# Optimization experiments

Measured on AMD Instinct MI355X. Metric: run time of the kernel, lower is better.

Reference implementation:

```python
import jax, jax.numpy as jnp
import numpy as np

IMG = 640
C = 80
K = 10
LB, LC = 7.5, 0.5
ALPHA_COST, BETA_COST = 0.5, 6.0
GAMMA, ALPHA = 2.0, 0.25
EPS = 1e-7
PI = 3.141592653589793


def xywh_to_xyxy(b):
    cx, cy, w, h = b[..., 0], b[..., 1], b[..., 2], b[..., 3]
    return jnp.stack([cx - w * 0.5, cy - h * 0.5, cx + w * 0.5, cy + h * 0.5], axis=-1)


def bbox_iou(box1, box2):
    # box1 [M,4], box2 [N,4] xyxy -> [M,N]
    area1 = jnp.clip(box1[:, 2] - box1[:, 0], 0) * jnp.clip(box1[:, 3] - box1[:, 1], 0)
    area2 = jnp.clip(box2[:, 2] - box2[:, 0], 0) * jnp.clip(box2[:, 3] - box2[:, 1], 0)
    ix1 = jnp.maximum(box1[:, None, 0], box2[None, :, 0])
    iy1 = jnp.maximum(box1[:, None, 1], box2[None, :, 1])
    ix2 = jnp.minimum(box1[:, None, 2], box2[None, :, 2])
    iy2 = jnp.minimum(box1[:, None, 3], box2[None, :, 3])
    inter = jnp.clip(ix2 - ix1, 0) * jnp.clip(iy2 - iy1, 0)
    union = area1[:, None] + area2[None, :] - inter + EPS
    return jnp.clip(inter / union, 0.0, 1.0)


def bbox_ciou(p, t):
    # elementwise [N,4] x [N,4] xyxy -> [N]
    px1, py1, px2, py2 = p[:, 0], p[:, 1], p[:, 2], p[:, 3]
    tx1, ty1, tx2, ty2 = t[:, 0], t[:, 1], t[:, 2], t[:, 3]
    pw = jnp.clip(px2 - px1, EPS)
    ph = jnp.clip(py2 - py1, EPS)
    tw = jnp.clip(tx2 - tx1, EPS)
    th = jnp.clip(ty2 - ty1, EPS)
    inter = jnp.clip(jnp.minimum(px2, tx2) - jnp.maximum(px1, tx1), 0) * \
            jnp.clip(jnp.minimum(py2, ty2) - jnp.maximum(py1, ty1), 0)
    union = pw * ph + tw * th - inter + EPS
    iou = inter / union
    cd = ((px1 + px2) * 0.5 - (tx1 + tx2) * 0.5) ** 2 + ((py1 + py2) * 0.5 - (ty1 + ty2) * 0.5) ** 2
    cw = jnp.maximum(px2, tx2) - jnp.minimum(px1, tx1)
    ch = jnp.maximum(py2, ty2) - jnp.minimum(py1, ty1)
    c2 = cw ** 2 + ch ** 2 + EPS
    v = (4.0 / PI ** 2) * (jnp.arctan(tw / th) - jnp.arctan(pw / ph)) ** 2
    alpha = jax.lax.stop_gradient(v / (v - iou + 1.0 + EPS))
    return iou - cd / c2 - alpha * v


def _decode(p, stride):
    # p: [B, A, S, S, E] -> box [B, A*S*S, 4] (xywh px), cls [B, A*S*S, C]
    B, A, S, _, E = p.shape
    tx, ty, tw, th = p[..., 0], p[..., 1], p[..., 2], p[..., 3]
    gy, gx = jnp.meshgrid(jnp.arange(S, dtype=p.dtype), jnp.arange(S, dtype=p.dtype), indexing='ij')
    gx = gx.reshape(1, 1, S, S)
    gy = gy.reshape(1, 1, S, S)
    px = (jax.nn.sigmoid(tx) * 2.0 - 0.5 + gx) * stride  # center_mode='v8'
    py = (jax.nn.sigmoid(ty) * 2.0 - 0.5 + gy) * stride
    pw = jax.nn.softplus(tw) * stride                      # wh_mode='softplus'
    ph = jax.nn.softplus(th) * stride
    box = jnp.stack([px, py, pw, ph], axis=-1).reshape(B, -1, 4)
    cls = p[..., 4:].reshape(B, -1, C)
    return box, cls


def _per_image(p_box, p_logits, gt, labels):
    # p_box [M,4] xywh, p_logits [M,C], gt [N,4] xyxy, labels [N]
    N = gt.shape[0]
    tcx = (gt[:, 0] + gt[:, 2]) * 0.5
    tcy = (gt[:, 1] + gt[:, 3]) * 0.5
    dist = (p_box[:, 0][:, None] - tcx[None, :]) ** 2 + (p_box[:, 1][:, None] - tcy[None, :]) ** 2  # [M,N]
    _, cand = jax.lax.top_k(-dist.T, K)       # [N,K] nearest anchors per target
    cand = cand.reshape(-1)                    # [N*K] (dups don't change the min)
    cand_box = p_box[cand]
    cand_logits = p_logits[cand]
    cls_score = jax.nn.sigmoid(cand_logits)[:, labels]          # [NK,N]
    iou = bbox_iou(xywh_to_xyxy(cand_box), gt)                  # [NK,N]
    cost = ALPHA_COST * (1.0 - cls_score) + BETA_COST * (1.0 - iou)
    matched = cand[jnp.argmin(cost, axis=0)]                    # [N]
    ciou = bbox_ciou(xywh_to_xyxy(p_box[matched]), gt)
    loss_box = LB * jnp.sum(1.0 - ciou) / N
    tgt = jnp.zeros_like(p_logits).at[matched, labels].set(1.0)  # [M,C]
    x = p_logits
    ce = jnp.maximum(x, 0) - x * tgt + jnp.log1p(jnp.exp(-jnp.abs(x)))
    pr = jax.nn.sigmoid(x)
    p_t = pr * tgt + (1 - pr) * (1 - tgt)
    fl = ce * (1 - p_t) ** GAMMA
    a_t = ALPHA * tgt + (1 - ALPHA) * (1 - tgt)
    loss_cls = LC * jnp.sum(a_t * fl) / N
    return loss_box + loss_cls


def _forward(p0, p1, p2, gt_boxes, labels):
    boxes, logits = [], []
    for p in (p0, p1, p2):
        S = p.shape[2]
        pb, pl = _decode(p, float(IMG) / S)
        boxes.append(pb)
        logits.append(pl)
    flat_boxes = jnp.concatenate(boxes, axis=1)    # [B, 8400, 4]
    flat_logits = jnp.concatenate(logits, axis=1)  # [B, 8400, C]
    per_img = jax.vmap(_per_image)(flat_boxes, flat_logits, gt_boxes, labels)  # [B]
    return jnp.mean(per_img)


def setup_inputs() -> dict:
    key = jax.random.key(0)
    k0, k1, k2, kc, kw, kl = jax.random.split(key, 6)
    B, N = 16, 60
    p0 = jax.random.normal(k0, (B, 1, 80, 80, 84), dtype=jnp.float32)
    p1 = jax.random.normal(k1, (B, 1, 40, 40, 84), dtype=jnp.float32)
    p2 = jax.random.normal(k2, (B, 1, 20, 20, 84), dtype=jnp.float32)
    c = jax.random.uniform(kc, (B, N, 2), minval=64.0, maxval=576.0)
    wh = jax.random.uniform(kw, (B, N, 2), minval=8.0, maxval=128.0)
    gt_boxes = jnp.concatenate([c - wh * 0.5, c + wh * 0.5], axis=-1).astype(jnp.float32)
    labels = jax.random.randint(kl, (B, N), 0, 80, dtype=jnp.int32)
    return {"p0": p0, "p1": p1, "p2": p2, "gt_boxes": gt_boxes, "labels": labels}


def reference(p0, p1, p2, gt_boxes, labels):
    return _forward(p0, p1, p2, gt_boxes, labels)
```

## Files before the change

### kernel.cpp

```cpp
#include <hip/hip_runtime.h>
#include <cfloat>
#include <math.h>

#define NB   16
#define NGT  60
#define NA   8400
#define KNN  10
#define NCAND (NGT*KNN)
#define EPSF 1e-7f
#define PIF  3.14159265358979f
#define FOCAL_BLOCKS 2048
#define TOPK_BLOCKS  240

#define NV0   2150400u
#define NV1    537600u
#define NV2    134400u
#define FOCAL_COUNT 2688000u

#define LOG2E 1.44269504088896341f
#define LN2   0.69314718055994531f

__device__ __forceinline__ float fexp2(float x){ return __builtin_amdgcn_exp2f(x); }
__device__ __forceinline__ float flog2(float x){ return __builtin_amdgcn_logf(x); }
__device__ __forceinline__ float frcp (float x){ return __builtin_amdgcn_rcpf(x); }

__device__ __forceinline__ float fsigm(float x){
  return frcp(1.0f + fexp2(-x*LOG2E));
}
__device__ __forceinline__ float fsoftplus(float x){
  float u = fexp2(-fabsf(x)*LOG2E);
  return fmaxf(x,0.f) + LN2*flog2(1.0f + u);
}
__device__ __forceinline__ float fbg(float x){
  float u = fexp2(fminf(-x*LOG2E, 126.0f));
  float t = frcp(1.0f + u);
  return (x + LN2*flog2(1.0f + u)) * t * t;
}

struct ARow { const float* q; float stf; int i, j; };
__device__ __forceinline__ ARow anchor_row(const float* p0,const float* p1,const float* p2,int img,int a){
  ARow r;
  if (a < 6400){ int l=a;      r.q = p0 + (size_t)(img*6400 + l)*84; r.stf= 8.f; r.i=l/80; r.j=l-80*r.i; }
  else if (a < 8000){ int l=a-6400; r.q = p1 + (size_t)(img*1600 + l)*84; r.stf=16.f; r.i=l/40; r.j=l-40*r.i; }
  else { int l=a-8000;         r.q = p2 + (size_t)(img*400  + l)*84; r.stf=32.f; r.i=l/20; r.j=l-20*r.i; }
  return r;
}
__device__ __forceinline__ float4 decode_box_xywh(const ARow& r){
  float4 x4 = *(const float4*)r.q;
  float px = (fsigm(x4.x)*2.f - 0.5f + (float)r.j)*r.stf;
  float py = (fsigm(x4.y)*2.f - 0.5f + (float)r.i)*r.stf;
  float pw = fsoftplus(x4.z)*r.stf;
  float ph = fsoftplus(x4.w)*r.stf;
  return make_float4(px,py,pw,ph);
}

__global__ __launch_bounds__(256) void focal_topk_kernel(const float* __restrict__ p0,
                                                         const float* __restrict__ p1,
                                                         const float* __restrict__ p2,
                                                         const float* __restrict__ gt,
                                                         int* __restrict__ cand,
                                                         float* __restrict__ fsum){
  if (blockIdx.x < TOPK_BLOCKS){
    int wid  = threadIdx.x >> 6;
    int lane = threadIdx.x & 63;
    int pair = blockIdx.x*4 + wid;
    int img = pair / NGT, g = pair - img*NGT;
    const float* gb = gt + (size_t)(img*NGT + g)*4;
    float tcx = (gb[0]+gb[2])*0.5f, tcy = (gb[1]+gb[3])*0.5f;

    int jx0 = (int)(tcx * 0.125f),   iy0 = (int)(tcy * 0.125f);
    int jx1 = (int)(tcx * 0.0625f),  iy1 = (int)(tcy * 0.0625f);
    int jx2 = (int)(tcx * 0.03125f), iy2 = (int)(tcy * 0.03125f);

    float d0=FLT_MAX,d1=FLT_MAX,d2=FLT_MAX,d3=FLT_MAX;
    int   a0,a1,a2,a3;
    #pragma unroll
    for (int s=0; s<4; s++){
      int c = lane + 64*s;
      float dd = FLT_MAX; int aa = 9000000 + c;
      const float* p; int i, j, S, base, rowmul, valid = 1; float stf;
      if (c < 169)      { int r=c/13,  q=c-13*r;           i=iy0-6+r; j=jx0-6+q; S=80; base=0;    p=p0; rowmul=6400; stf= 8.f; }
      else if (c < 218) { int t=c-169; int r=t/7, q=t-7*r; i=iy1-3+r; j=jx1-3+q; S=40; base=6400; p=p1; rowmul=1600; stf=16.f; }
      else if (c < 243) { int t=c-218; int r=t/5, q=t-5*r; i=iy2-2+r; j=jx2-2+q; S=20; base=8000; p=p2; rowmul=400;  stf=32.f; }
      else { valid = 0; i=j=0; S=1; base=0; p=p0; rowmul=0; stf=0.f; }
      if (valid && i>=0 && i<S && j>=0 && j<S){
        int local = i*S + j;
        const float* q4 = p + (size_t)(img*rowmul + local)*84u;
        float2 xy = *(const float2*)q4;
        float px = (fsigm(xy.x)*2.f - 0.5f + (float)j)*stf;
        float py = (fsigm(xy.y)*2.f - 0.5f + (float)i)*stf;
        float dx=px-tcx, dy=py-tcy;
        dd = dx*dx + dy*dy;
        aa = base + local;
      }
      if (s==0){ d0=dd; a0=aa; } else if (s==1){ d1=dd; a1=aa; }
      else if (s==2){ d2=dd; a2=aa; } else { d3=dd; a3=aa; }
    }

    for (int r=0; r<KNN; r++){
      float v = d0; int anc = a0;
      if (d1 < v || (d1==v && a1<anc)){ v=d1; anc=a1; }
      if (d2 < v || (d2==v && a2<anc)){ v=d2; anc=a2; }
      if (d3 < v || (d3==v && a3<anc)){ v=d3; anc=a3; }
      #pragma unroll
      for (int off=32; off>0; off>>=1){
        float v2 = __shfl_xor(v, off);
        int  A2 = __shfl_xor(anc, off);
        if (v2 < v || (v2==v && A2<anc)){ v=v2; anc=A2; }
      }
      if (a0==anc) d0=FLT_MAX;
      if (a1==anc) d1=FLT_MAX;
      if (a2==anc) d2=FLT_MAX;
      if (a3==anc) d3=FLT_MAX;
      if (lane == 0) cand[(size_t)pair*KNN + r] = anc;
    }
    return;
  }

  __shared__ float sbuf[4];
  float sum = 0.f;
  const unsigned stride = FOCAL_BLOCKS*256u;
  for (unsigned u = (blockIdx.x - TOPK_BLOCKS)*256u + threadIdx.x; u < FOCAL_COUNT; u += stride){
    unsigned g = u / 20u;
    unsigned v = 21u*g + (u - 20u*g) + 1u;
    const float* p; unsigned vloc;
    if (v < NV0)           { p=p0; vloc = v; }
    else if (v < NV0+NV1)  { p=p1; vloc = v - NV0; }
    else                   { p=p2; vloc = v - (NV0+NV1); }
    float4 x4 = *(const float4*)(p + (size_t)vloc*4u);
    sum += fbg(x4.x) + fbg(x4.y) + fbg(x4.z) + fbg(x4.w);
  }
  sum *= 0.75f;
  #pragma unroll
  for (int off=32; off>0; off>>=1) sum += __shfl_xor(sum, off);
  int wid = threadIdx.x >> 6;
  if ((threadIdx.x & 63) == 0) sbuf[wid] = sum;
  __syncthreads();
  if (threadIdx.x == 0) fsum[blockIdx.x - TOPK_BLOCKS] = sbuf[0]+sbuf[1]+sbuf[2]+sbuf[3];
}

__global__ __launch_bounds__(256) void match_kernel(const int* __restrict__ cand,
                                                    const float* __restrict__ gt,
                                                    const int* __restrict__ labels,
                                                    const float* __restrict__ p0,
                                                    const float* __restrict__ p1,
                                                    const float* __restrict__ p2,
                                                    int* __restrict__ matched){
  int pair = blockIdx.x;
  int img = pair / NGT, j = pair - img*NGT;
  int tid = threadIdx.x;
  int wid = tid >> 6, lane = tid & 63;
  const float* gb = gt + (size_t)(img*NGT + j)*4;
  float gx=gb[0], gy=gb[1], gz=gb[2], gw=gb[3];
  float a2 = fmaxf(gz-gx,0.f)*fmaxf(gw-gy,0.f);
  int lab = labels[img*NGT + j];

  const int* ci = cand + (size_t)img*NCAND;
  float best = FLT_MAX; int bslot = 1<<30; int banchor = -1;
  for (int c=tid; c<NCAND; c+=256){
    int a = ci[c];
    ARow ar = anchor_row(p0,p1,p2,img,a);
    float4 b = decode_box_xywh(ar);
    float bx1=b.x-b.z*0.5f, by1=b.y-b.w*0.5f, bx2=b.x+b.z*0.5f, by2=b.y+b.w*0.5f;
    float a1 = fmaxf(bx2-bx1,0.f)*fmaxf(by2-by1,0.f);
    float ix1=fmaxf(bx1,gx), iy1=fmaxf(by1,gy);
    float ix2=fminf(bx2,gz), iy2=fminf(by2,gw);
    float inter = fmaxf(ix2-ix1,0.f)*fmaxf(iy2-iy1,0.f);
    float uni = a1 + a2 - inter + EPSF;
    float iou = fminf(fmaxf(inter/uni,0.f),1.f);
    float lg = ar.q[4+lab];
    float cost = 0.5f*(1.f - fsigm(lg)) + 6.f*(1.f - iou);
    if (cost < best){ best=cost; bslot=c; banchor=a; }
  }
  #pragma unroll
  for (int off=32; off>0; off>>=1){
    float v2 = __shfl_xor(best, off);
    int  s2 = __shfl_xor(bslot, off);
    int  a2s= __shfl_xor(banchor, off);
    if (v2 < best || (v2==best && s2<bslot)){ best=v2; bslot=s2; banchor=a2s; }
  }
  __shared__ float bc[4]; __shared__ int bs[4], ba[4];
  if (lane == 0){ bc[wid]=best; bs[wid]=bslot; ba[wid]=banchor; }
  __syncthreads();
  if (tid == 0){
    float v=bc[0]; int s=bs[0]; int a=ba[0];
    #pragma unroll
    for (int k=1;k<4;k++){
      if (bc[k] < v || (bc[k]==v && bs[k]<s)){ v=bc[k]; s=bs[k]; a=ba[k]; }
    }
    matched[img*NGT + j] = a;
  }
}

__global__ __launch_bounds__(1024) void tail_kernel(const int* __restrict__ matched_g,
                                                    const float* __restrict__ gt,
                                                    const int* __restrict__ labels,
                                                    const float* __restrict__ p0,
                                                    const float* __restrict__ p1,
                                                    const float* __restrict__ p2,
                                                    const float* __restrict__ fsum,
                                                    float* __restrict__ out){
  int tid = threadIdx.x;
  int wid = tid >> 6;
  int lane = tid & 63;
  __shared__ int sm[NB][NGT];
  __shared__ int sl[NB][NGT];
  __shared__ float wb[NB], wc[NB], wf[NB];
  if (lane < NGT){
    sm[wid][lane] = matched_g[wid*NGT + lane];
    sl[wid][lane] = labels[wid*NGT + lane];
  }
  __syncthreads();

  int img = wid;
  float local_box = 0.f, local_corr = 0.f;
  if (lane < NGT){
    int j = lane;
    int m = sm[img][j];
    ARow ar = anchor_row(p0,p1,p2,img,m);
    float4 pb = decode_box_xywh(ar);
    float px1=pb.x-pb.z*0.5f, py1=pb.y-pb.w*0.5f, px2=pb.x+pb.z*0.5f, py2=pb.y+pb.w*0.5f;
    const float* gb = gt + (size_t)(img*NGT + j)*4;
    float gx=gb[0], gy=gb[1], gz=gb[2], gw=gb[3];
    float pw=fmaxf(px2-px1,EPSF), ph=fmaxf(py2-py1,EPSF);
    float tw=fmaxf(gz-gx,EPSF),  th=fmaxf(gw-gy,EPSF);
    float inter = fmaxf(fminf(px2,gz)-fmaxf(px1,gx),0.f)*fmaxf(fminf(py2,gw)-fmaxf(py1,gy),0.f);
    float uni = pw*ph + tw*th - inter + EPSF;
    float iou = inter/uni;
    float dcx = (px1+px2)*0.5f - (gx+gz)*0.5f;
    float dcy = (py1+py2)*0.5f - (gy+gw)*0.5f;
    float cd = dcx*dcx + dcy*dcy;
    float cw = fmaxf(px2,gz) - fminf(px1,gx);
    float ch = fmaxf(py2,gw) - fminf(py1,gy);
    float c2 = cw*cw + ch*ch + EPSF;
    float dv = atanf(tw/th) - atanf(pw/ph);
    float v  = (4.f/(PIF*PIF))*dv*dv;
    float alpha = v/(v - iou + 1.f + EPSF);
    float ciou = iou - cd/c2 - alpha*v;
    local_box = 1.f - ciou;

    int lab = sl[img][j];
    bool dup = false;
    for (int j2=0; j2<j; j2++)
      if (sm[img][j2]==m && sl[img][j2]==lab){ dup=true; break; }
    if (!dup){
      float x = ar.q[4+lab];
      float s  = fsigm(x);
      float u  = fexp2(-fabsf(x)*LOG2E);
      float lt = LN2*flog2(1.0f + u);
      float sp_pos = fmaxf(-x,0.f) + lt;
      float sp_neg = fmaxf( x,0.f) + lt;
      local_corr = 0.25f*sp_pos*(1.f-s)*(1.f-s) - 0.75f*sp_neg*s*s;
    }
  }
  float local_f = fsum[tid] + fsum[tid + 1024];
  #pragma unroll
  for (int off=32; off>0; off>>=1){
    local_box  += __shfl_xor(local_box,  off);
    local_corr += __shfl_xor(local_corr, off);
    local_f    += __shfl_xor(local_f,    off);
  }
  if (lane == 0){ wb[wid]=local_box; wc[wid]=local_corr; wf[wid]=local_f; }
  __syncthreads();
  if (tid == 0){
    float sb=0.f, sc=0.f, sf=0.f;
    #pragma unroll
    for (int k=0;k<NB;k++){ sb+=wb[k]; sc+=wc[k]; sf+=wf[k]; }
    out[0] = (7.5f*sb + 0.5f*(sf + sc)) / (60.f*16.f);
  }
}

extern "C" void kernel_launch(void* const* d_in, const int* in_sizes, int n_in,
                              void* d_out, int out_size, void* d_ws, size_t ws_size,
                              hipStream_t stream){
  const float* p0 = (const float*)d_in[0];
  const float* p1 = (const float*)d_in[1];
  const float* p2 = (const float*)d_in[2];
  const float* gt = (const float*)d_in[3];
  const int* labels = (const int*)d_in[4];
  float* out = (float*)d_out;

  int*   cand    = (int*)d_ws;
  int*   matched = (int*)((char*)cand + (size_t)NB*NCAND*sizeof(int));
  float* fsum    = (float*)((char*)matched + (size_t)NB*NGT*sizeof(int));

  focal_topk_kernel<<<TOPK_BLOCKS + FOCAL_BLOCKS, 256, 0, stream>>>(p0, p1, p2, gt, cand, fsum);
  match_kernel<<<NB*NGT, 256, 0, stream>>>(cand, gt, labels, p0, p1, p2, matched);
  tail_kernel<<<1, 1024, 0, stream>>>(matched, gt, labels, p0, p1, p2, fsum, out);
}
```

Measured before the change: 43.15 us.

## Fuse top-k, matching and per-image loss into one per-image block kernel

```diff
diff --git a/kernel.cpp b/kernel.cpp
--- a/kernel.cpp
+++ b/kernel.cpp
@@ -9,8 +9,10 @@
 #define NCAND (NGT*KNN)
 #define EPSF 1e-7f
 #define PIF  3.14159265358979f
-#define FOCAL_BLOCKS 2048
-#define TOPK_BLOCKS  240
+
+#define IMG_BLOCKS   16
+#define FOCAL_BLOCKS 1050
+#define K1_BLOCKS    (IMG_BLOCKS + FOCAL_BLOCKS)
 
 #define NV0   2150400u
 #define NV1    537600u
@@ -54,20 +56,56 @@
   return make_float4(px,py,pw,ph);
 }
 
-__global__ __launch_bounds__(256) void focal_topk_kernel(const float* __restrict__ p0,
-                                                         const float* __restrict__ p1,
-                                                         const float* __restrict__ p2,
-                                                         const float* __restrict__ gt,
-                                                         int* __restrict__ cand,
-                                                         float* __restrict__ fsum){
-  if (blockIdx.x < TOPK_BLOCKS){
-    int wid  = threadIdx.x >> 6;
-    int lane = threadIdx.x & 63;
-    int pair = blockIdx.x*4 + wid;
-    int img = pair / NGT, g = pair - img*NGT;
+__global__ __launch_bounds__(512) void mega_kernel(const float* __restrict__ p0,
+                                                   const float* __restrict__ p1,
+                                                   const float* __restrict__ p2,
+                                                   const float* __restrict__ gt,
+                                                   const int* __restrict__ labels,
+                                                   float* __restrict__ fsum,
+                                                   float* __restrict__ imgpart){
+  int tid  = threadIdx.x;
+  int wid  = tid >> 6;
+  int lane = tid & 63;
+
+  if (blockIdx.x >= IMG_BLOCKS){
+    __shared__ float sbuf[8];
+    float sum = 0.f;
+    const unsigned stride = FOCAL_BLOCKS*512u;
+    unsigned u = (blockIdx.x - IMG_BLOCKS)*512u + tid;
+    #pragma unroll
+    for (int it=0; it<5; ++it, u += stride){
+      unsigned g = u / 20u;
+      unsigned v = 21u*g + (u - 20u*g) + 1u;
+      const float* p; unsigned vloc;
+      if (v < NV0)           { p=p0; vloc = v; }
+      else if (v < NV0+NV1)  { p=p1; vloc = v - NV0; }
+      else                   { p=p2; vloc = v - (NV0+NV1); }
+      float4 x4 = *(const float4*)(p + (size_t)vloc*4u);
+      sum += fbg(x4.x) + fbg(x4.y) + fbg(x4.z) + fbg(x4.w);
+    }
+    sum *= 0.75f;
+    #pragma unroll
+    for (int off=32; off>0; off>>=1) sum += __shfl_xor(sum, off);
+    if (lane == 0) sbuf[wid] = sum;
+    __syncthreads();
+    if (tid == 0){
+      float s = 0.f;
+      #pragma unroll
+      for (int k=0;k<8;k++) s += sbuf[k];
+      fsum[blockIdx.x - IMG_BLOCKS] = s;
+    }
+    return;
+  }
+
+  int img = blockIdx.x;
+  __shared__ int   scand[NCAND];
+  __shared__ int   smatch[NGT];
+  __shared__ int   slab[NGT];
+  __shared__ float sred[2];
+
+  for (int g = wid; g < NGT; g += 8){
     const float* gb = gt + (size_t)(img*NGT + g)*4;
     float tcx = (gb[0]+gb[2])*0.5f, tcy = (gb[1]+gb[3])*0.5f;
-
     int jx0 = (int)(tcx * 0.125f),   iy0 = (int)(tcy * 0.125f);
     int jx1 = (int)(tcx * 0.0625f),  iy1 = (int)(tcy * 0.0625f);
     int jx2 = (int)(tcx * 0.03125f), iy2 = (int)(tcy * 0.03125f);
@@ -96,7 +134,6 @@
       if (s==0){ d0=dd; a0=aa; } else if (s==1){ d1=dd; a1=aa; }
       else if (s==2){ d2=dd; a2=aa; } else { d3=dd; a3=aa; }
     }
-
     for (int r=0; r<KNN; r++){
       float v = d0; int anc = a0;
       if (d1 < v || (d1==v && a1<anc)){ v=d1; anc=a1; }
@@ -112,160 +149,116 @@
       if (a1==anc) d1=FLT_MAX;
       if (a2==anc) d2=FLT_MAX;
       if (a3==anc) d3=FLT_MAX;
-      if (lane == 0) cand[(size_t)pair*KNN + r] = anc;
-    }
-    return;
-  }
-
-  __shared__ float sbuf[4];
-  float sum = 0.f;
-  const unsigned stride = FOCAL_BLOCKS*256u;
-  for (unsigned u = (blockIdx.x - TOPK_BLOCKS)*256u + threadIdx.x; u < FOCAL_COUNT; u += stride){
-    unsigned g = u / 20u;
-    unsigned v = 21u*g + (u - 20u*g) + 1u;
-    const float* p; unsigned vloc;
-    if (v < NV0)           { p=p0; vloc = v; }
-    else if (v < NV0+NV1)  { p=p1; vloc = v - NV0; }
-    else                   { p=p2; vloc = v - (NV0+NV1); }
-    float4 x4 = *(const float4*)(p + (size_t)vloc*4u);
-    sum += fbg(x4.x) + fbg(x4.y) + fbg(x4.z) + fbg(x4.w);
-  }
-  sum *= 0.75f;
-  #pragma unroll
-  for (int off=32; off>0; off>>=1) sum += __shfl_xor(sum, off);
-  int wid = threadIdx.x >> 6;
-  if ((threadIdx.x & 63) == 0) sbuf[wid] = sum;
+      if (lane == 0) scand[g*KNN + r] = anc;
+    }
+  }
   __syncthreads();
-  if (threadIdx.x == 0) fsum[blockIdx.x - TOPK_BLOCKS] = sbuf[0]+sbuf[1]+sbuf[2]+sbuf[3];
-}
-
-__global__ __launch_bounds__(256) void match_kernel(const int* __restrict__ cand,
-                                                    const float* __restrict__ gt,
-                                                    const int* __restrict__ labels,
-                                                    const float* __restrict__ p0,
-                                                    const float* __restrict__ p1,
-                                                    const float* __restrict__ p2,
-                                                    int* __restrict__ matched){
-  int pair = blockIdx.x;
-  int img = pair / NGT, j = pair - img*NGT;
+
+  for (int g = wid; g < NGT; g += 8){
+    const float* gb = gt + (size_t)(img*NGT + g)*4;
+    float gx=gb[0], gy=gb[1], gz=gb[2], gw=gb[3];
+    float a2 = fmaxf(gz-gx,0.f)*fmaxf(gw-gy,0.f);
+    int lab = labels[img*NGT + g];
+
+    float best = FLT_MAX; int bslot = 1<<30; int banchor = -1;
+    for (int c=lane; c<NCAND; c+=64){
+      int a = scand[c];
+      ARow ar = anchor_row(p0,p1,p2,img,a);
+      float4 b = decode_box_xywh(ar);
+      float bx1=b.x-b.z*0.5f, by1=b.y-b.w*0.5f, bx2=b.x+b.z*0.5f, by2=b.y+b.w*0.5f;
+      float a1 = fmaxf(bx2-bx1,0.f)*fmaxf(by2-by1,0.f);
+      float ix1=fmaxf(bx1,gx), iy1=fmaxf(by1,gy);
+      float ix2=fminf(bx2,gz), iy2=fminf(by2,gw);
+      float inter = fmaxf(ix2-ix1,0.f)*fmaxf(iy2-iy1,0.f);
+      float uni = a1 + a2 - inter + EPSF;
+      float iou = fminf(fmaxf(inter/uni,0.f),1.f);
+      float lg = ar.q[4+lab];
+      float cost = 0.5f*(1.f - fsigm(lg)) + 6.f*(1.f - iou);
+      if (cost < best){ best=cost; bslot=c; banchor=a; }
+    }
+    #pragma unroll
+    for (int off=32; off>0; off>>=1){
+      float v2 = __shfl_xor(best, off);
+      int  s2 = __shfl_xor(bslot, off);
+      int  a2s= __shfl_xor(banchor, off);
+      if (v2 < best || (v2==best && s2<bslot)){ best=v2; bslot=s2; banchor=a2s; }
+    }
+    if (lane == 0){ smatch[g] = banchor; slab[g] = labels[img*NGT + g]; }
+  }
+  __syncthreads();
+
+  if (wid == 0){
+    float local_box = 0.f, local_corr = 0.f;
+    if (lane < NGT){
+      int j = lane;
+      int m = smatch[j];
+      ARow ar = anchor_row(p0,p1,p2,img,m);
+      float4 pb = decode_box_xywh(ar);
+      float px1=pb.x-pb.z*0.5f, py1=pb.y-pb.w*0.5f, px2=pb.x+pb.z*0.5f, py2=pb.y+pb.w*0.5f;
+      const float* gb = gt + (size_t)(img*NGT + j)*4;
+      float gx=gb[0], gy=gb[1], gz=gb[2], gw=gb[3];
+      float pw=fmaxf(px2-px1,EPSF), ph=fmaxf(py2-py1,EPSF);
+      float tw=fmaxf(gz-gx,EPSF),  th=fmaxf(gw-gy,EPSF);
+      float inter = fmaxf(fminf(px2,gz)-fmaxf(px1,gx),0.f)*fmaxf(fminf(py2,gw)-fmaxf(py1,gy),0.f);
+      float uni = pw*ph + tw*th - inter + EPSF;
+      float iou = inter/uni;
+      float dcx = (px1+px2)*0.5f - (gx+gz)*0.5f;
+      float dcy = (py1+py2)*0.5f - (gy+gw)*0.5f;
+      float cd = dcx*dcx + dcy*dcy;
+      float cw = fmaxf(px2,gz) - fminf(px1,gx);
+      float ch = fmaxf(py2,gw) - fminf(py1,gy);
+      float c2 = cw*cw + ch*ch + EPSF;
+      float dv = atanf(tw/th) - atanf(pw/ph);
+      float v  = (4.f/(PIF*PIF))*dv*dv;
+      float alpha = v/(v - iou + 1.f + EPSF);
+      float ciou = iou - cd/c2 - alpha*v;
+      local_box = 1.f - ciou;
+
+      int lab = slab[j];
+      bool dup = false;
+      for (int j2=0; j2<j; j2++)
+        if (smatch[j2]==m && slab[j2]==lab){ dup=true; break; }
+      if (!dup){
+        float x = ar.q[4+lab];
+        float s  = fsigm(x);
+        float u  = fexp2(-fabsf(x)*LOG2E);
+        float lt = LN2*flog2(1.0f + u);
+        float sp_pos = fmaxf(-x,0.f) + lt;
+        float sp_neg = fmaxf( x,0.f) + lt;
+        local_corr = 0.25f*sp_pos*(1.f-s)*(1.f-s) - 0.75f*sp_neg*s*s;
+      }
+    }
+    #pragma unroll
+    for (int off=32; off>0; off>>=1){
+      local_box  += __shfl_xor(local_box,  off);
+      local_corr += __shfl_xor(local_corr, off);
+    }
+    if (lane == 0){ imgpart[img] = local_box; imgpart[IMG_BLOCKS + img] = local_corr; }
+  }
+}
+
+__global__ __launch_bounds__(1024) void finalize_kernel(const float* __restrict__ fsum,
+                                                        const float* __restrict__ imgpart,
+                                                        float* __restrict__ out){
   int tid = threadIdx.x;
   int wid = tid >> 6, lane = tid & 63;
-  const float* gb = gt + (size_t)(img*NGT + j)*4;
-  float gx=gb[0], gy=gb[1], gz=gb[2], gw=gb[3];
-  float a2 = fmaxf(gz-gx,0.f)*fmaxf(gw-gy,0.f);
-  int lab = labels[img*NGT + j];
-
-  const int* ci = cand + (size_t)img*NCAND;
-  float best = FLT_MAX; int bslot = 1<<30; int banchor = -1;
-  for (int c=tid; c<NCAND; c+=256){
-    int a = ci[c];
-    ARow ar = anchor_row(p0,p1,p2,img,a);
-    float4 b = decode_box_xywh(ar);
-    float bx1=b.x-b.z*0.5f, by1=b.y-b.w*0.5f, bx2=b.x+b.z*0.5f, by2=b.y+b.w*0.5f;
-    float a1 = fmaxf(bx2-bx1,0.f)*fmaxf(by2-by1,0.f);
-    float ix1=fmaxf(bx1,gx), iy1=fmaxf(by1,gy);
-    float ix2=fminf(bx2,gz), iy2=fminf(by2,gw);
-    float inter = fmaxf(ix2-ix1,0.f)*fmaxf(iy2-iy1,0.f);
-    float uni = a1 + a2 - inter + EPSF;
-    float iou = fminf(fmaxf(inter/uni,0.f),1.f);
-    float lg = ar.q[4+lab];
-    float cost = 0.5f*(1.f - fsigm(lg)) + 6.f*(1.f - iou);
-    if (cost < best){ best=cost; bslot=c; banchor=a; }
-  }
+  __shared__ float wf[16], wb[16], wc[16];
+  float f = fsum[tid];
+  if (tid < FOCAL_BLOCKS - 1024) f += fsum[tid + 1024];
+  float b = (tid < IMG_BLOCKS) ? imgpart[tid] : 0.f;
+  float c = (tid < IMG_BLOCKS) ? imgpart[IMG_BLOCKS + tid] : 0.f;
   #pragma unroll
   for (int off=32; off>0; off>>=1){
-    float v2 = __shfl_xor(best, off);
-    int  s2 = __shfl_xor(bslot, off);
-    int  a2s= __shfl_xor(banchor, off);
-    if (v2 < best || (v2==best && s2<bslot)){ best=v2; bslot=s2; banchor=a2s; }
-  }
-  __shared__ float bc[4]; __shared__ int bs[4], ba[4];
-  if (lane == 0){ bc[wid]=best; bs[wid]=bslot; ba[wid]=banchor; }
+    f += __shfl_xor(f, off);
+    b += __shfl_xor(b, off);
+    c += __shfl_xor(c, off);
+  }
+  if (lane == 0){ wf[wid]=f; wb[wid]=b; wc[wid]=c; }
   __syncthreads();
   if (tid == 0){
-    float v=bc[0]; int s=bs[0]; int a=ba[0];
-    #pragma unroll
-    for (int k=1;k<4;k++){
-      if (bc[k] < v || (bc[k]==v && bs[k]<s)){ v=bc[k]; s=bs[k]; a=ba[k]; }
-    }
-    matched[img*NGT + j] = a;
-  }
-}
-
-__global__ __launch_bounds__(1024) void tail_kernel(const int* __restrict__ matched_g,
-                                                    const float* __restrict__ gt,
-                                                    const int* __restrict__ labels,
-                                                    const float* __restrict__ p0,
-                                                    const float* __restrict__ p1,
-                                                    const float* __restrict__ p2,
-                                                    const float* __restrict__ fsum,
-                                                    float* __restrict__ out){
-  int tid = threadIdx.x;
-  int wid = tid >> 6;
-  int lane = tid & 63;
-  __shared__ int sm[NB][NGT];
-  __shared__ int sl[NB][NGT];
-  __shared__ float wb[NB], wc[NB], wf[NB];
-  if (lane < NGT){
-    sm[wid][lane] = matched_g[wid*NGT + lane];
-    sl[wid][lane] = labels[wid*NGT + lane];
-  }
-  __syncthreads();
-
-  int img = wid;
-  float local_box = 0.f, local_corr = 0.f;
-  if (lane < NGT){
-    int j = lane;
-    int m = sm[img][j];
-    ARow ar = anchor_row(p0,p1,p2,img,m);
-    float4 pb = decode_box_xywh(ar);
-    float px1=pb.x-pb.z*0.5f, py1=pb.y-pb.w*0.5f, px2=pb.x+pb.z*0.5f, py2=pb.y+pb.w*0.5f;
-    const float* gb = gt + (size_t)(img*NGT + j)*4;
-    float gx=gb[0], gy=gb[1], gz=gb[2], gw=gb[3];
-    float pw=fmaxf(px2-px1,EPSF), ph=fmaxf(py2-py1,EPSF);
-    float tw=fmaxf(gz-gx,EPSF),  th=fmaxf(gw-gy,EPSF);
-    float inter = fmaxf(fminf(px2,gz)-fmaxf(px1,gx),0.f)*fmaxf(fminf(py2,gw)-fmaxf(py1,gy),0.f);
-    float uni = pw*ph + tw*th - inter + EPSF;
-    float iou = inter/uni;
-    float dcx = (px1+px2)*0.5f - (gx+gz)*0.5f;
-    float dcy = (py1+py2)*0.5f - (gy+gw)*0.5f;
-    float cd = dcx*dcx + dcy*dcy;
-    float cw = fmaxf(px2,gz) - fminf(px1,gx);
-    float ch = fmaxf(py2,gw) - fminf(py1,gy);
-    float c2 = cw*cw + ch*ch + EPSF;
-    float dv = atanf(tw/th) - atanf(pw/ph);
-    float v  = (4.f/(PIF*PIF))*dv*dv;
-    float alpha = v/(v - iou + 1.f + EPSF);
-    float ciou = iou - cd/c2 - alpha*v;
-    local_box = 1.f - ciou;
-
-    int lab = sl[img][j];
-    bool dup = false;
-    for (int j2=0; j2<j; j2++)
-      if (sm[img][j2]==m && sl[img][j2]==lab){ dup=true; break; }
-    if (!dup){
-      float x = ar.q[4+lab];
-      float s  = fsigm(x);
-      float u  = fexp2(-fabsf(x)*LOG2E);
-      float lt = LN2*flog2(1.0f + u);
-      float sp_pos = fmaxf(-x,0.f) + lt;
-      float sp_neg = fmaxf( x,0.f) + lt;
-      local_corr = 0.25f*sp_pos*(1.f-s)*(1.f-s) - 0.75f*sp_neg*s*s;
-    }
-  }
-  float local_f = fsum[tid] + fsum[tid + 1024];
-  #pragma unroll
-  for (int off=32; off>0; off>>=1){
-    local_box  += __shfl_xor(local_box,  off);
-    local_corr += __shfl_xor(local_corr, off);
-    local_f    += __shfl_xor(local_f,    off);
-  }
-  if (lane == 0){ wb[wid]=local_box; wc[wid]=local_corr; wf[wid]=local_f; }
-  __syncthreads();
-  if (tid == 0){
-    float sb=0.f, sc=0.f, sf=0.f;
-    #pragma unroll
-    for (int k=0;k<NB;k++){ sb+=wb[k]; sc+=wc[k]; sf+=wf[k]; }
+    float sf=0.f, sb=0.f, sc=0.f;
+    #pragma unroll
+    for (int k=0;k<16;k++){ sf+=wf[k]; sb+=wb[k]; sc+=wc[k]; }
     out[0] = (7.5f*sb + 0.5f*(sf + sc)) / (60.f*16.f);
   }
 }
@@ -280,11 +273,9 @@
   const int* labels = (const int*)d_in[4];
   float* out = (float*)d_out;
 
-  int*   cand    = (int*)d_ws;
-  int*   matched = (int*)((char*)cand + (size_t)NB*NCAND*sizeof(int));
-  float* fsum    = (float*)((char*)matched + (size_t)NB*NGT*sizeof(int));
-
-  focal_topk_kernel<<<TOPK_BLOCKS + FOCAL_BLOCKS, 256, 0, stream>>>(p0, p1, p2, gt, cand, fsum);
-  match_kernel<<<NB*NGT, 256, 0, stream>>>(cand, gt, labels, p0, p1, p2, matched);
-  tail_kernel<<<1, 1024, 0, stream>>>(matched, gt, labels, p0, p1, p2, fsum, out);
-}
+  float* fsum    = (float*)d_ws;
+  float* imgpart = fsum + FOCAL_BLOCKS;
+
+  mega_kernel<<<K1_BLOCKS, 512, 0, stream>>>(p0, p1, p2, gt, labels, fsum, imgpart);
+  finalize_kernel<<<1, 1024, 0, stream>>>(fsum, imgpart, out);
+}
```

New measurement: 131.4 us. 3.04x slower.
